# Kernel optimization log

Hardware: AMD Instinct MI355X
Metric: run time of the kernel (lower is better)

## Reference

```python
import jax, jax.numpy as jnp
import numpy as np
from jax import lax

B, C, H, W = 4, 256, 64, 64
NH, DK, DV = 8, 32, 32
KER, PAD = 3, 1


def conv1x1(x, w, b=None):
    # x: [B,C,H,W], w: [O,C] (1x1 conv kernel), b: [O] or None
    y = jnp.einsum('bchw,oc->bohw', x, w)
    if b is not None:
        y = y + b[None, :, None, None]
    return y


def unfold(x, k, pad):
    # F.unfold equivalent: [B,C,H,W] -> [B, C*k*k, H, W] (channel-major patch order)
    return lax.conv_general_dilated_patches(x, (k, k), (1, 1), [(pad, pad), (pad, pad)])


def local_attention(q, k, v, kernel, pad, n_head):
    # per-head local windowed attention over a kernel x kernel neighborhood
    b, c, h, w = q.shape
    d = c // n_head
    kk = kernel * kernel
    qh = q.reshape(b, n_head, d, h, w)
    kpat = unfold(k, kernel, pad).reshape(b, n_head, d, kk, h, w)
    vpat = unfold(v, kernel, pad).reshape(b, n_head, d, kk, h, w)
    scale = 1.0 / np.sqrt(float(d)).astype(np.float32)
    logits = jnp.einsum('bhdxy,bhdkxy->bhkxy', qh, kpat) * scale
    attn = jax.nn.softmax(logits, axis=2)
    out = jnp.einsum('bhkxy,bhdkxy->bhdxy', attn, vpat)
    return out.reshape(b, c, h, w)


def layernorm2d(x, g, b, eps=1e-6):
    mu = jnp.mean(x, axis=1, keepdims=True)
    var = jnp.mean((x - mu) ** 2, axis=1, keepdims=True)
    return (x - mu) / jnp.sqrt(var + eps) * g[None, :, None, None] + b[None, :, None, None]


def batchnorm2d(x, g, b, eps=1e-5):
    mu = jnp.mean(x, axis=(0, 2, 3), keepdims=True)
    var = jnp.mean((x - mu) ** 2, axis=(0, 2, 3), keepdims=True)
    return (x - mu) / jnp.sqrt(var + eps) * g[None, :, None, None] + b[None, :, None, None]


def mha(xq, xkv, wq, wk, wv, wfc, g, bias, kernel, pad):
    residual = xq
    q = conv1x1(xq, wq)
    k = conv1x1(xkv, wk)
    v = conv1x1(xkv, wv)
    o = local_attention(q, k, v, kernel, pad, NH)
    o = conv1x1(o, wfc) + residual
    return layernorm2d(o, g, bias)


def ffn(x, w1, b1, w2, b2, g, bias):
    residual = x
    y = conv1x1(jax.nn.relu(conv1x1(x, w1, b1)), w2, b2)
    y = batchnorm2d(y, g, bias)
    return y + residual


def setup_inputs() -> dict:
    key = jax.random.key(0)
    ks = jax.random.split(key, 16)
    s = 0.05
    d = {
        'input1': jax.random.normal(ks[0], (B, C, H, W), jnp.float32),
        'input2': jax.random.normal(ks[1], (B, C, H, W), jnp.float32),
        'slf_wq': jax.random.normal(ks[2], (NH * DK, C), jnp.float32) * s,
        'slf_wk': jax.random.normal(ks[3], (NH * DK, C), jnp.float32) * s,
        'slf_wv': jax.random.normal(ks[4], (NH * DV, C), jnp.float32) * s,
        'slf_fc': jax.random.normal(ks[5], (C, NH * DV), jnp.float32) * s,
        'slf_g': jnp.ones((C,), jnp.float32),
        'slf_b': jnp.zeros((C,), jnp.float32),
        'crs_wq': jax.random.normal(ks[6], (NH * DK, C), jnp.float32) * s,
        'crs_wk': jax.random.normal(ks[7], (NH * DK, C), jnp.float32) * s,
        'crs_wv': jax.random.normal(ks[8], (NH * DV, C), jnp.float32) * s,
        'crs_fc': jax.random.normal(ks[9], (C, NH * DV), jnp.float32) * s,
        'crs_g': jnp.ones((C,), jnp.float32),
        'crs_b': jnp.zeros((C,), jnp.float32),
        'ffn_w1': jax.random.normal(ks[10], (C, C), jnp.float32) * s,
        'ffn_b1': jnp.zeros((C,), jnp.float32),
        'ffn_w2': jax.random.normal(ks[11], (C, C), jnp.float32) * s,
        'ffn_b2': jnp.zeros((C,), jnp.float32),
        'ffn_bn_g': jnp.ones((C,), jnp.float32),
        'ffn_bn_b': jnp.zeros((C,), jnp.float32),
        'kernel': KER,
        'pad': PAD,
    }
    return d


def reference(input1, input2, slf_wq, slf_wk, slf_wv, slf_fc, slf_g, slf_b,
              crs_wq, crs_wk, crs_wv, crs_fc, crs_g, crs_b,
              ffn_w1, ffn_b1, ffn_w2, ffn_b2, ffn_bn_g, ffn_bn_b, kernel, pad):
    slf1 = mha(input1, input1, slf_wq, slf_wk, slf_wv, slf_fc, slf_g, slf_b, kernel, pad)
    slf2 = mha(input2, input2, slf_wq, slf_wk, slf_wv, slf_fc, slf_g, slf_b, kernel, pad)
    crs1 = mha(slf1, slf2, crs_wq, crs_wk, crs_wv, crs_fc, crs_g, crs_b, kernel, pad)
    crs2 = mha(slf2, slf1, crs_wq, crs_wk, crs_wv, crs_fc, crs_g, crs_b, kernel, pad)
    out1 = ffn(crs1, ffn_w1, ffn_b1, ffn_w2, ffn_b2, ffn_bn_g, ffn_bn_b)
    out2 = ffn(crs2, ffn_w1, ffn_b1, ffn_w2, ffn_b2, ffn_bn_g, ffn_bn_b)
    return (out1, out2)
```

## Files before the change

### kernel.cpp

```cpp
#include <hip/hip_runtime.h>
#include <stdint.h>

using u16 = unsigned short;
typedef __bf16 bf16x8 __attribute__((ext_vector_type(8)));
typedef __bf16 bf16x2 __attribute__((ext_vector_type(2)));
typedef float f32x4 __attribute__((ext_vector_type(4)));

#define NPIX 16384
#define CDIM 256

__device__ __forceinline__ float b2f(u16 u) {
  union { unsigned i; float f; } c; c.i = ((unsigned)u) << 16; return c.f;
}
__device__ __forceinline__ u16 f2b(float x) {
  union { __bf16 h; u16 u; } c; c.h = (__bf16)x; return c.u;
}
__device__ __forceinline__ unsigned pack2(float a, float b) {
  union { bf16x2 v; unsigned u; } c; c.v[0] = (__bf16)a; c.v[1] = (__bf16)b; return c.u;
}
__device__ __forceinline__ void unpack8(uint4 w, float* f) {
  f[0] = b2f((u16)(w.x & 0xffffu)); f[1] = b2f((u16)(w.x >> 16));
  f[2] = b2f((u16)(w.y & 0xffffu)); f[3] = b2f((u16)(w.y >> 16));
  f[4] = b2f((u16)(w.z & 0xffffu)); f[5] = b2f((u16)(w.z >> 16));
  f[6] = b2f((u16)(w.w & 0xffffu)); f[7] = b2f((u16)(w.w >> 16));
}

__device__ __forceinline__ void async16(u16* l, const u16* g) {
  __builtin_amdgcn_global_load_lds((const __attribute__((address_space(1))) void*)g,
                                   (__attribute__((address_space(3))) void*)l, 16, 0, 0);
}

template <int NI, int NT>
__device__ __forceinline__ void stage_swz(u16* lds, const u16* src, int tid) {
#pragma unroll
  for (int i = 0; i < NI; ++i) {
    const int idx = i * NT + tid;
    const int row = idx >> 3;
    const int c8 = (idx & 7) ^ (row & 7);
    async16(lds + idx * 8, src + (size_t)row * 256 + c8 * 8);
  }
}

__device__ __forceinline__ void compute_tile(const u16* ab, const u16* bb,
                                             f32x4 (&acc)[4][4], int wr, int wc,
                                             int l15, int l4, int sw) {
#pragma unroll
  for (int kk = 0; kk < 2; ++kk) {
    const int cs = ((kk * 4 + l4) ^ sw) * 8;
    bf16x8 af[4], bfr[4];
#pragma unroll
    for (int mi = 0; mi < 4; ++mi)
      af[mi] = *(const bf16x8*)&ab[(wr * 64 + mi * 16 + l15) * 64 + cs];
#pragma unroll
    for (int ni = 0; ni < 4; ++ni)
      bfr[ni] = *(const bf16x8*)&bb[(wc * 64 + ni * 16 + l15) * 64 + cs];
#pragma unroll
    for (int mi = 0; mi < 4; ++mi)
#pragma unroll
      for (int ni = 0; ni < 4; ++ni)
        acc[mi][ni] = __builtin_amdgcn_mfma_f32_16x16x32_bf16(af[mi], bfr[ni],
                                                              acc[mi][ni], 0, 0, 0);
  }
}

__global__ void prep(const float* __restrict__ x1, const float* __restrict__ x2,
                     u16* __restrict__ X1, u16* __restrict__ X2,
                     const float* s0, const float* s1, const float* s2,
                     const float* s3, const float* s4, const float* s5,
                     const float* s6, const float* s7, const float* s8,
                     const float* s9, u16* __restrict__ wdst,
                     float* __restrict__ stats) {
  const int t = threadIdx.x;
  const int yy = blockIdx.y;
  if (yy >= 32) {
    const int m = yy - 32;
    if (m == 0 && blockIdx.x == 0) {
      ((float4*)stats)[t] = float4{0.f, 0.f, 0.f, 0.f};
    }
    const float* s;
    switch (m) {
      case 0: s = s0; break; case 1: s = s1; break; case 2: s = s2; break;
      case 3: s = s3; break; case 4: s = s4; break; case 5: s = s5; break;
      case 6: s = s6; break; case 7: s = s7; break; case 8: s = s8; break;
      default: s = s9; break;
    }
    const int i = (blockIdx.x * 256 + t) * 4;
    float4 v = *(const float4*)(s + i);
    uint2 o;
    o.x = pack2(v.x, v.y);
    o.y = pack2(v.z, v.w);
    *(uint2*)(wdst + (size_t)m * 65536 + i) = o;
    return;
  }
  __shared__ u16 tile[64][65];
  const int z = yy >> 2;
  const float* x = (z < 4) ? x1 : x2;
  u16* X = (z < 4) ? X1 : X2;
  const int b = z & 3, c0 = (yy & 3) * 64, hw0 = blockIdx.x * 64;
  {
    const int hw_l = t & 63, cb = t >> 6;
#pragma unroll
    for (int i = 0; i < 16; ++i) {
      const int c_l = cb * 16 + i;
      tile[c_l][hw_l] = f2b(x[((size_t)(b * 256 + c0 + c_l)) * 4096 + hw0 + hw_l]);
    }
  }
  __syncthreads();
  {
    const int c_l = t & 63, hb = t >> 6;
#pragma unroll
    for (int i = 0; i < 16; ++i) {
      const int hw_l = hb * 16 + i;
      X[((size_t)(b * 4096 + hw0 + hw_l)) * 256 + c0 + c_l] = tile[c_l][hw_l];
    }
  }
}

struct PG { const u16* X[6]; const u16* W[3]; u16* D[6]; };

template <int NG>
__global__ void gemm_qkv(PG a) {
  __shared__ u16 As[2][8192];
  __shared__ u16 Bs[2][8192];
  const int tid = threadIdx.x;
  const int wave = tid >> 6, lane = tid & 63;
  const int p0 = blockIdx.x * 128;
  const int g = blockIdx.y >> 1, o0 = (blockIdx.y & 1) * 128;
  const int z = blockIdx.z;
  const u16* X = a.X[z * NG + g];
  const u16* W = a.W[g];
  u16* D = a.D[z * NG + g];
  const int wr = wave & 1, wc = wave >> 1;
  const int l15 = lane & 15, l4 = lane >> 4;
  const int sw = l15 & 7;
  f32x4 acc[4][4] = {};

  const u16* Xp = X + (size_t)p0 * 256;
  const u16* Wp = W + (size_t)o0 * 256;
  stage_swz<4, 256>(As[0], Xp, tid);
  stage_swz<4, 256>(Bs[0], Wp, tid);
  __syncthreads();

  for (int kt = 0; kt < 4; ++kt) {
    const int cur = kt & 1;
    if (kt < 3) {
      stage_swz<4, 256>(As[cur ^ 1], Xp + (kt + 1) * 64, tid);
      stage_swz<4, 256>(Bs[cur ^ 1], Wp + (kt + 1) * 64, tid);
    }
    compute_tile(As[cur], Bs[cur], acc, wr, wc, l15, l4, sw);
    __syncthreads();
  }
#pragma unroll
  for (int ni = 0; ni < 4; ++ni) {
    const int o = o0 + wc * 64 + ni * 16 + l15;
#pragma unroll
    for (int mi = 0; mi < 4; ++mi)
#pragma unroll
      for (int r = 0; r < 4; ++r) {
        const int p = p0 + wr * 64 + mi * 16 + l4 * 4 + r;
        D[(size_t)p * 256 + o] = f2b(acc[mi][ni][r]);
      }
  }
}

struct Pas { const u16* Q[2]; const u16* K[2]; const u16* V[2];
             const u16* res[2]; u16* dstS[2]; u16* dstQc[2];
             const u16* Wfc; const u16* Wcq; const float* g; const float* b; };

__global__ __launch_bounds__(512) void attn_s(Pas a) {
  __shared__ u16 A4[2][8192];
  __shared__ u16 Bs[16384];
  __shared__ u16 S4[4][8192];
  __shared__ float red[2][128][4];
  const int tid = threadIdx.x;
  const int wave = tid >> 6, lane = tid & 63;
  const int wr = wave & 1, wc = wave >> 1;
  const int l15 = lane & 15, l4 = lane >> 4;
  const int sw = l15 & 7;
  const int p0 = blockIdx.x * 128;
  const int z = blockIdx.y;
  const u16* __restrict__ Q = a.Q[z];
  const u16* __restrict__ K = a.K[z];
  const u16* __restrict__ V = a.V[z];
  const u16* __restrict__ res = a.res[z];
  u16* dstS = a.dstS[z];
  u16* dstQc = a.dstQc[z];

  const int p_l = tid >> 2, hh = tid & 3;
  const int p = p0 + p_l;
  const int yq = (p >> 6) & 63, xq = p & 63;

  bool inb[9];
  ptrdiff_t noff[9];
#pragma unroll
  for (int j = 0; j < 9; ++j) {
    const int dy = j / 3 - 1, dx = j % 3 - 1;
    inb[j] = ((unsigned)(yq + dy) < 64u) && ((unsigned)(xq + dx) < 64u);
    noff[j] = (ptrdiff_t)(dy * 64 + dx) * 256;
  }

  stage_swz<4, 512>(Bs, a.Wfc, tid);
  __builtin_amdgcn_sched_barrier(0);

  f32x4 acc[4][4] = {};
  for (int h = 0; h < 2; ++h) {
    const int head = h * 4 + hh;
    const size_t base = (size_t)p * 256 + head * 32;
    float q[32];
    {
      const uint4* qp = (const uint4*)(Q + base);
#pragma unroll
      for (int i = 0; i < 4; ++i) { uint4 w = qp[i]; unpack8(w, q + i * 8); }
    }
    float accj[9];
#pragma unroll
    for (int j = 0; j < 9; ++j) accj[j] = 0.f;
#pragma unroll
    for (int i = 0; i < 4; ++i) {
      uint4 w[9];
#pragma unroll
      for (int j = 0; j < 9; ++j)
        if (inb[j]) w[j] = ((const uint4*)(K + base + noff[j]))[i];
#pragma unroll
      for (int j = 0; j < 9; ++j) {
        if (inb[j]) {
          float kf[8]; unpack8(w[j], kf);
#pragma unroll
          for (int d = 0; d < 8; ++d) accj[j] += q[i * 8 + d] * kf[d];
        }
      }
    }
    float lg[9];
    float mx = -1e30f;
#pragma unroll
    for (int j = 0; j < 9; ++j) {
      const float l = inb[j] ? accj[j] * 0.17677669529663687f : 0.f;
      lg[j] = l;
      mx = fmaxf(mx, l);
    }
    float pr[9], den = 0.f;
#pragma unroll
    for (int j = 0; j < 9; ++j) { pr[j] = __expf(lg[j] - mx); den += pr[j]; }
    float out[32];
#pragma unroll
    for (int d = 0; d < 32; ++d) out[d] = 0.f;
#pragma unroll
    for (int i = 0; i < 4; ++i) {
      uint4 w[9];
#pragma unroll
      for (int j = 0; j < 9; ++j)
        if (inb[j]) w[j] = ((const uint4*)(V + base + noff[j]))[i];
#pragma unroll
      for (int j = 0; j < 9; ++j) {
        if (inb[j]) {
          float vf[8]; unpack8(w[j], vf);
          const float pw = pr[j];
#pragma unroll
          for (int d = 0; d < 8; ++d) out[i * 8 + d] += pw * vf[d];
        }
      }
    }
    const float inv = 1.f / den;
#pragma unroll
    for (int i = 0; i < 4; ++i) {
      uint4 w;
      w.x = pack2(out[i * 8 + 0] * inv, out[i * 8 + 1] * inv);
      w.y = pack2(out[i * 8 + 2] * inv, out[i * 8 + 3] * inv);
      w.z = pack2(out[i * 8 + 4] * inv, out[i * 8 + 5] * inv);
      w.w = pack2(out[i * 8 + 6] * inv, out[i * 8 + 7] * inv);
      const int c8g = hh * 4 + i;
      const int sub = c8g >> 3, c8in = c8g & 7;
      *(uint4*)&A4[sub][p_l * 64 + ((c8in ^ (p_l & 7)) * 8)] = w;
    }

    __syncthreads();
    compute_tile(A4[0], Bs, acc, wr, wc, l15, l4, sw);
    __syncthreads();
    stage_swz<4, 512>(Bs, a.Wfc + (h * 2 + 1) * 64, tid);
    __syncthreads();
    compute_tile(A4[1], Bs, acc, wr, wc, l15, l4, sw);
    __syncthreads();
    if (h == 0) {
      stage_swz<4, 512>(Bs, a.Wfc + 2 * 64, tid);
      __builtin_amdgcn_sched_barrier(0);
    }
  }

  stage_swz<4, 512>(Bs, a.Wcq, tid);
  __builtin_amdgcn_sched_barrier(0);

#pragma unroll
  for (int mi = 0; mi < 4; ++mi) {
#pragma unroll
    for (int r = 0; r < 4; ++r) {
      const int pl = wr * 64 + mi * 16 + l4 * 4 + r;
      const int pp = p0 + pl;
      float s = 0.f, s2 = 0.f;
#pragma unroll
      for (int ni = 0; ni < 4; ++ni) {
        const int o = wc * 64 + ni * 16 + l15;
        float vv = acc[mi][ni][r] + b2f(res[(size_t)pp * 256 + o]);
        acc[mi][ni][r] = vv;
        s += vv; s2 += vv * vv;
      }
#pragma unroll
      for (int m = 1; m < 16; m <<= 1) {
        s += __shfl_xor(s, m); s2 += __shfl_xor(s2, m);
      }
      if (l15 == 0) { red[0][pl][wc] = s; red[1][pl][wc] = s2; }
    }
  }
  __syncthreads();

  float gv[4], bv[4];
#pragma unroll
  for (int ni = 0; ni < 4; ++ni) {
    const int o = wc * 64 + ni * 16 + l15;
    gv[ni] = a.g[o]; bv[ni] = a.b[o];
  }
#pragma unroll
  for (int mi = 0; mi < 4; ++mi) {
#pragma unroll
    for (int r = 0; r < 4; ++r) {
      const int pl = wr * 64 + mi * 16 + l4 * 4 + r;
      const float st = red[0][pl][0] + red[0][pl][1] + red[0][pl][2] + red[0][pl][3];
      const float s2t = red[1][pl][0] + red[1][pl][1] + red[1][pl][2] + red[1][pl][3];
      const float mu = st * (1.f / 256.f);
      const float var = s2t * (1.f / 256.f) - mu * mu;
      const float inv = rsqrtf(var + 1e-6f);
      const int pp = p0 + pl;
#pragma unroll
      for (int ni = 0; ni < 4; ++ni) {
        const int o = wc * 64 + ni * 16 + l15;
        const u16 hv = f2b((acc[mi][ni][r] - mu) * inv * gv[ni] + bv[ni]);
        dstS[(size_t)pp * 256 + o] = hv;
        const int c8 = (ni * 16 + l15) >> 3;
        S4[wc][pl * 64 + ((c8 ^ (pl & 7)) * 8) + (l15 & 7)] = hv;
      }
    }
  }
  __syncthreads();

  u16* a4f = &A4[0][0];
  f32x4 accq[4][4] = {};
  for (int kt = 0; kt < 4; ++kt) {
    if (kt < 3)
      stage_swz<4, 512>(((kt + 1) & 1) ? a4f : Bs, a.Wcq + (kt + 1) * 64, tid);
    compute_tile(&S4[kt][0], (kt & 1) ? a4f : Bs, accq, wr, wc, l15, l4, sw);
    __syncthreads();
  }
#pragma unroll
  for (int ni = 0; ni < 4; ++ni) {
    const int o = wc * 64 + ni * 16 + l15;
#pragma unroll
    for (int mi = 0; mi < 4; ++mi)
#pragma unroll
      for (int r = 0; r < 4; ++r) {
        const int pp = p0 + wr * 64 + mi * 16 + l4 * 4 + r;
        dstQc[(size_t)pp * 256 + o] = f2b(accq[mi][ni][r]);
      }
  }
}

struct Pcf { const u16* Q[2]; const u16* K[2]; const u16* V[2];
             const u16* resS[2]; u16* dstC[2]; u16* U[2]; float* st[2];
             const u16* Wfc; const float* g; const float* b;
             const u16* W1; const float* bb1; const u16* W2; const float* bb2; };

__global__ __launch_bounds__(512) void attn_c_ffn(Pcf a) {
  __shared__ u16 A4[2][8192];
  __shared__ u16 Bs[16384];
  __shared__ u16 M4[4][8192];
  __shared__ float red[2][128][4];
  const int tid = threadIdx.x;
  const int wave = tid >> 6, lane = tid & 63;
  const int wr = wave & 1, wc = wave >> 1;
  const int l15 = lane & 15, l4 = lane >> 4;
  const int sw = l15 & 7;
  const int p0 = blockIdx.x * 128;
  const int z = blockIdx.y;
  const u16* __restrict__ Q = a.Q[z];
  const u16* __restrict__ K = a.K[z];
  const u16* __restrict__ V = a.V[z];
  const u16* __restrict__ resS = a.resS[z];
  u16* dstC = a.dstC[z];
  u16* U = a.U[z];
  float* st = a.st[z];

  const int p_l = tid >> 2, hh = tid & 3;
  const int p = p0 + p_l;
  const int yq = (p >> 6) & 63, xq = p & 63;

  bool inb[9];
  ptrdiff_t noff[9];
#pragma unroll
  for (int j = 0; j < 9; ++j) {
    const int dy = j / 3 - 1, dx = j % 3 - 1;
    inb[j] = ((unsigned)(yq + dy) < 64u) && ((unsigned)(xq + dx) < 64u);
    noff[j] = (ptrdiff_t)(dy * 64 + dx) * 256;
  }

  stage_swz<4, 512>(Bs, a.Wfc, tid);
  __builtin_amdgcn_sched_barrier(0);

  f32x4 acc[4][4] = {};
  for (int h = 0; h < 2; ++h) {
    const int head = h * 4 + hh;
    const size_t base = (size_t)p * 256 + head * 32;
    float q[32];
    {
      const uint4* qp = (const uint4*)(Q + base);
#pragma unroll
      for (int i = 0; i < 4; ++i) { uint4 w = qp[i]; unpack8(w, q + i * 8); }
    }
    float accj[9];
#pragma unroll
    for (int j = 0; j < 9; ++j) accj[j] = 0.f;
#pragma unroll
    for (int i = 0; i < 4; ++i) {
      uint4 w[9];
#pragma unroll
      for (int j = 0; j < 9; ++j)
        if (inb[j]) w[j] = ((const uint4*)(K + base + noff[j]))[i];
#pragma unroll
      for (int j = 0; j < 9; ++j) {
        if (inb[j]) {
          float kf[8]; unpack8(w[j], kf);
#pragma unroll
          for (int d = 0; d < 8; ++d) accj[j] += q[i * 8 + d] * kf[d];
        }
      }
    }
    float lg[9];
    float mx = -1e30f;
#pragma unroll
    for (int j = 0; j < 9; ++j) {
      const float l = inb[j] ? accj[j] * 0.17677669529663687f : 0.f;
      lg[j] = l;
      mx = fmaxf(mx, l);
    }
    float pr[9], den = 0.f;
#pragma unroll
    for (int j = 0; j < 9; ++j) { pr[j] = __expf(lg[j] - mx); den += pr[j]; }
    float out[32];
#pragma unroll
    for (int d = 0; d < 32; ++d) out[d] = 0.f;
#pragma unroll
    for (int i = 0; i < 4; ++i) {
      uint4 w[9];
#pragma unroll
      for (int j = 0; j < 9; ++j)
        if (inb[j]) w[j] = ((const uint4*)(V + base + noff[j]))[i];
#pragma unroll
      for (int j = 0; j < 9; ++j) {
        if (inb[j]) {
          float vf[8]; unpack8(w[j], vf);
          const float pw = pr[j];
#pragma unroll
          for (int d = 0; d < 8; ++d) out[i * 8 + d] += pw * vf[d];
        }
      }
    }
    const float inv = 1.f / den;
#pragma unroll
    for (int i = 0; i < 4; ++i) {
      uint4 w;
      w.x = pack2(out[i * 8 + 0] * inv, out[i * 8 + 1] * inv);
      w.y = pack2(out[i * 8 + 2] * inv, out[i * 8 + 3] * inv);
      w.z = pack2(out[i * 8 + 4] * inv, out[i * 8 + 5] * inv);
      w.w = pack2(out[i * 8 + 6] * inv, out[i * 8 + 7] * inv);
      const int c8g = hh * 4 + i;
      const int sub = c8g >> 3, c8in = c8g & 7;
      *(uint4*)&A4[sub][p_l * 64 + ((c8in ^ (p_l & 7)) * 8)] = w;
    }

    __syncthreads();
    compute_tile(A4[0], Bs, acc, wr, wc, l15, l4, sw);
    __syncthreads();
    stage_swz<4, 512>(Bs, a.Wfc + (h * 2 + 1) * 64, tid);
    __syncthreads();
    compute_tile(A4[1], Bs, acc, wr, wc, l15, l4, sw);
    __syncthreads();
    if (h == 0) {
      stage_swz<4, 512>(Bs, a.Wfc + 2 * 64, tid);
      __builtin_amdgcn_sched_barrier(0);
    }
  }

  stage_swz<4, 512>(Bs, a.W1, tid);
  __builtin_amdgcn_sched_barrier(0);

#pragma unroll
  for (int mi = 0; mi < 4; ++mi) {
#pragma unroll
    for (int r = 0; r < 4; ++r) {
      const int pl = wr * 64 + mi * 16 + l4 * 4 + r;
      const int pp = p0 + pl;
      float s = 0.f, s2 = 0.f;
#pragma unroll
      for (int ni = 0; ni < 4; ++ni) {
        const int o = wc * 64 + ni * 16 + l15;
        float vv = acc[mi][ni][r] + b2f(resS[(size_t)pp * 256 + o]);
        acc[mi][ni][r] = vv;
        s += vv; s2 += vv * vv;
      }
#pragma unroll
      for (int m = 1; m < 16; m <<= 1) {
        s += __shfl_xor(s, m); s2 += __shfl_xor(s2, m);
      }
      if (l15 == 0) { red[0][pl][wc] = s; red[1][pl][wc] = s2; }
    }
  }
  __syncthreads();

  float gv[4], bv[4];
#pragma unroll
  for (int ni = 0; ni < 4; ++ni) {
    const int o = wc * 64 + ni * 16 + l15;
    gv[ni] = a.g[o]; bv[ni] = a.b[o];
  }
#pragma unroll
  for (int mi = 0; mi < 4; ++mi) {
#pragma unroll
    for (int r = 0; r < 4; ++r) {
      const int pl = wr * 64 + mi * 16 + l4 * 4 + r;
      const float st2 = red[0][pl][0] + red[0][pl][1] + red[0][pl][2] + red[0][pl][3];
      const float s2t = red[1][pl][0] + red[1][pl][1] + red[1][pl][2] + red[1][pl][3];
      const float mu = st2 * (1.f / 256.f);
      const float var = s2t * (1.f / 256.f) - mu * mu;
      const float inv = rsqrtf(var + 1e-6f);
      const int pp = p0 + pl;
#pragma unroll
      for (int ni = 0; ni < 4; ++ni) {
        const int o = wc * 64 + ni * 16 + l15;
        const u16 hv = f2b((acc[mi][ni][r] - mu) * inv * gv[ni] + bv[ni]);
        dstC[(size_t)pp * 256 + o] = hv;
        const int c8 = (ni * 16 + l15) >> 3;
        M4[wc][pl * 64 + ((c8 ^ (pl & 7)) * 8) + (l15 & 7)] = hv;
      }
    }
  }
  __syncthreads();

  u16* a4f = &A4[0][0];
  f32x4 acc1[4][4] = {};
  for (int kt = 0; kt < 4; ++kt) {
    if (kt < 3)
      stage_swz<4, 512>(((kt + 1) & 1) ? a4f : Bs, a.W1 + (kt + 1) * 64, tid);
    compute_tile(&M4[kt][0], (kt & 1) ? a4f : Bs, acc1, wr, wc, l15, l4, sw);
    __syncthreads();
  }
  stage_swz<4, 512>(Bs, a.W2, tid);
  __builtin_amdgcn_sched_barrier(0);
  {
    float bvv[4];
#pragma unroll
    for (int ni = 0; ni < 4; ++ni) bvv[ni] = a.bb1[wc * 64 + ni * 16 + l15];
    u16* ml = &M4[wc][0];
#pragma unroll
    for (int mi = 0; mi < 4; ++mi) {
#pragma unroll
      for (int r = 0; r < 4; ++r) {
        const int pl = wr * 64 + mi * 16 + l4 * 4 + r;
#pragma unroll
        for (int ni = 0; ni < 4; ++ni) {
          const int col = ni * 16 + l15;
          const int c8 = col >> 3;
          const u16 hv = f2b(fmaxf(acc1[mi][ni][r] + bvv[ni], 0.f));
          ml[pl * 64 + ((c8 ^ (pl & 7)) * 8) + (col & 7)] = hv;
        }
      }
    }
  }
  __syncthreads();

  f32x4 acc2[4][4] = {};
  for (int kt = 0; kt < 4; ++kt) {
    if (kt < 3)
      stage_swz<4, 512>(((kt + 1) & 1) ? a4f : Bs, a.W2 + (kt + 1) * 64, tid);
    compute_tile(&M4[kt][0], (kt & 1) ? a4f : Bs, acc2, wr, wc, l15, l4, sw);
    __syncthreads();
  }
#pragma unroll
  for (int ni = 0; ni < 4; ++ni) {
    const int o = wc * 64 + ni * 16 + l15;
    const float bvv = a.bb2[o];
    float s = 0.f, s2 = 0.f;
#pragma unroll
    for (int mi = 0; mi < 4; ++mi) {
#pragma unroll
      for (int r = 0; r < 4; ++r) {
        const int pp = p0 + wr * 64 + mi * 16 + l4 * 4 + r;
        const u16 hv = f2b(acc2[mi][ni][r] + bvv);
        U[(size_t)pp * 256 + o] = hv;
        const float vr = b2f(hv); s += vr; s2 += vr * vr;
      }
    }
    s += __shfl_xor(s, 16); s2 += __shfl_xor(s2, 16);
    s += __shfl_xor(s, 32); s2 += __shfl_xor(s2, 32);
    if (l4 == 0) { atomicAdd(&st[o], s); atomicAdd(&st[256 + o], s2); }
  }
}

struct Pbn { const u16* U[2]; const u16* res[2]; const float* st[2];
             float* out[2]; const float* g; const float* b; };

__global__ void bn_apply(Pbn a) {
  __shared__ float tile[64][65];
  const int t = threadIdx.x;
  const int s = blockIdx.z >> 2, b = blockIdx.z & 3;
  const u16* __restrict__ U = a.U[s];
  const u16* __restrict__ res = a.res[s];
  const float* st = a.st[s];
  float* out = a.out[s];
  const int c0 = blockIdx.y * 64, hw0 = blockIdx.x * 64;
  {
    const int c_l = t & 63, hb = t >> 6;
    const int c = c0 + c_l;
    const float mu = st[c] * (1.f / 16384.f);
    const float var = st[256 + c] * (1.f / 16384.f) - mu * mu;
    const float sc = rsqrtf(var + 1e-5f) * a.g[c];
    const float sh = a.b[c] - mu * sc;
#pragma unroll
    for (int i = 0; i < 16; ++i) {
      const int hw_l = hb * 16 + i;
      const size_t p = (size_t)b * 4096 + hw0 + hw_l;
      const float u = b2f(U[p * 256 + c]);
      const float r = b2f(res[p * 256 + c]);
      tile[hw_l][c_l] = u * sc + sh + r;
    }
  }
  __syncthreads();
  {
    const int hw_l = t & 63, cb2 = t >> 6;
#pragma unroll
    for (int i = 0; i < 16; ++i) {
      const int c_l = cb2 * 16 + i;
      out[((size_t)(b * 256 + c0 + c_l)) * 4096 + hw0 + hw_l] = tile[hw_l][c_l];
    }
  }
}

extern "C" void kernel_launch(void* const* d_in, const int* in_sizes, int n_in,
                              void* d_out, int out_size, void* d_ws, size_t ws_size,
                              hipStream_t stream) {
  const float* input1 = (const float*)d_in[0];
  const float* input2 = (const float*)d_in[1];
  const float* slf_wq = (const float*)d_in[2];
  const float* slf_wk = (const float*)d_in[3];
  const float* slf_wv = (const float*)d_in[4];
  const float* slf_fc = (const float*)d_in[5];
  const float* slf_g  = (const float*)d_in[6];
  const float* slf_b  = (const float*)d_in[7];
  const float* crs_wq = (const float*)d_in[8];
  const float* crs_wk = (const float*)d_in[9];
  const float* crs_wv = (const float*)d_in[10];
  const float* crs_fc = (const float*)d_in[11];
  const float* crs_g  = (const float*)d_in[12];
  const float* crs_b  = (const float*)d_in[13];
  const float* ffn_w1 = (const float*)d_in[14];
  const float* ffn_b1 = (const float*)d_in[15];
  const float* ffn_w2 = (const float*)d_in[16];
  const float* ffn_b2 = (const float*)d_in[17];
  const float* bn_g   = (const float*)d_in[18];
  const float* bn_b   = (const float*)d_in[19];

  float* out = (float*)d_out;
  u16* ws = (u16*)d_ws;
  const size_t TS = (size_t)NPIX * CDIM;
  u16* b[10];
  for (int i = 0; i < 10; ++i) b[i] = ws + (size_t)i * TS;
  u16* wb = ws + 10 * TS;
  u16 *Wsq = wb,             *Wsk = wb + 65536,     *Wsv = wb + 2 * 65536,
      *Wsf = wb + 3 * 65536, *Wcq = wb + 4 * 65536, *Wck = wb + 5 * 65536,
      *Wcv = wb + 6 * 65536, *Wcf = wb + 7 * 65536, *W1 = wb + 8 * 65536,
      *W2 = wb + 9 * 65536;
  float* stats = (float*)(wb + 10 * 65536);

  const dim3 tb(256);

  prep<<<dim3(64, 42), tb, 0, stream>>>(input1, input2, b[0], b[1],
                                        slf_wq, slf_wk, slf_wv, slf_fc,
                                        crs_wq, crs_wk, crs_wv, crs_fc,
                                        ffn_w1, ffn_w2, wb, stats);

  PG sa;
  sa.X[0] = b[0]; sa.X[1] = b[0]; sa.X[2] = b[0];
  sa.X[3] = b[1]; sa.X[4] = b[1]; sa.X[5] = b[1];
  sa.W[0] = Wsq; sa.W[1] = Wsk; sa.W[2] = Wsv;
  sa.D[0] = b[4]; sa.D[1] = b[5]; sa.D[2] = b[6];
  sa.D[3] = b[7]; sa.D[4] = b[8]; sa.D[5] = b[9];
  gemm_qkv<3><<<dim3(NPIX / 128, 6, 2), tb, 0, stream>>>(sa);

  Pas f1;
  f1.Q[0] = b[4]; f1.K[0] = b[5]; f1.V[0] = b[6];
  f1.Q[1] = b[7]; f1.K[1] = b[8]; f1.V[1] = b[9];
  f1.res[0] = b[0]; f1.res[1] = b[1];
  f1.dstS[0] = b[2]; f1.dstS[1] = b[3];
  f1.dstQc[0] = b[4]; f1.dstQc[1] = b[7];
  f1.Wfc = Wsf; f1.Wcq = Wcq; f1.g = slf_g; f1.b = slf_b;
  attn_s<<<dim3(NPIX / 128, 2), dim3(512), 0, stream>>>(f1);

  PG ca;
  ca.X[0] = b[2]; ca.X[1] = b[2];
  ca.X[2] = b[3]; ca.X[3] = b[3];
  ca.X[4] = nullptr; ca.X[5] = nullptr;
  ca.W[0] = Wck; ca.W[1] = Wcv; ca.W[2] = nullptr;
  ca.D[0] = b[5]; ca.D[1] = b[6];
  ca.D[2] = b[8]; ca.D[3] = b[9];
  ca.D[4] = nullptr; ca.D[5] = nullptr;
  gemm_qkv<2><<<dim3(NPIX / 128, 4, 2), tb, 0, stream>>>(ca);

  Pcf f2;
  f2.Q[0] = b[4]; f2.K[0] = b[8]; f2.V[0] = b[9];
  f2.Q[1] = b[7]; f2.K[1] = b[5]; f2.V[1] = b[6];
  f2.resS[0] = b[2]; f2.resS[1] = b[3];
  f2.dstC[0] = b[0]; f2.dstC[1] = b[1];
  f2.U[0] = b[2]; f2.U[1] = b[3];
  f2.st[0] = stats; f2.st[1] = stats + 512;
  f2.Wfc = Wcf; f2.g = crs_g; f2.b = crs_b;
  f2.W1 = W1; f2.bb1 = ffn_b1; f2.W2 = W2; f2.bb2 = ffn_b2;
  attn_c_ffn<<<dim3(NPIX / 128, 2), dim3(512), 0, stream>>>(f2);

  Pbn bn;
  bn.U[0] = b[2]; bn.U[1] = b[3];
  bn.res[0] = b[0]; bn.res[1] = b[1];
  bn.st[0] = stats; bn.st[1] = stats + 512;
  bn.out[0] = out; bn.out[1] = out + TS;
  bn.g = bn_g; bn.b = bn_b;
  bn_apply<<<dim3(64, 4, 8), tb, 0, stream>>>(bn);
}
```

Baseline: 283.0 us.

## Fuse cross-attention K/V projections into self-attention epilogue kernel

The self-attention kernel already keeps its layernormed output tile in shared memory to compute the cross-attention Q projection. It now also computes the cross-attention K and V projections from that same tile, running the weight staging pipeline across all three weight matrices. This removes the separate gemm_qkv launch for cross K/V, which re-read the self-attention outputs from global memory. The cost is more work per attention block, plus two extra workspace buffers and a reshuffled buffer assignment; whether the original input buffers are free to overwrite in attn_s depends on no other reads of them there.

```diff
diff --git a/kernel.cpp b/kernel.cpp
--- a/kernel.cpp
+++ b/kernel.cpp
@@ -165,7 +165,9 @@
 
 struct Pas { const u16* Q[2]; const u16* K[2]; const u16* V[2];
              const u16* res[2]; u16* dstS[2]; u16* dstQc[2];
-             const u16* Wfc; const u16* Wcq; const float* g; const float* b; };
+             u16* dstKc[2]; u16* dstVc[2];
+             const u16* Wfc; const u16* Wcq; const u16* Wck; const u16* Wcv;
+             const float* g; const float* b; };
 
 __global__ __launch_bounds__(512) void attn_s(Pas a) {
   __shared__ u16 A4[2][8192];
@@ -184,7 +186,6 @@
   const u16* __restrict__ V = a.V[z];
   const u16* __restrict__ res = a.res[z];
   u16* dstS = a.dstS[z];
-  u16* dstQc = a.dstQc[z];
 
   const int p_l = tid >> 2, hh = tid & 3;
   const int p = p0 + p_l;
@@ -342,23 +343,33 @@
   __syncthreads();
 
   u16* a4f = &A4[0][0];
-  f32x4 accq[4][4] = {};
-  for (int kt = 0; kt < 4; ++kt) {
-    if (kt < 3)
-      stage_swz<4, 512>(((kt + 1) & 1) ? a4f : Bs, a.Wcq + (kt + 1) * 64, tid);
-    compute_tile(&S4[kt][0], (kt & 1) ? a4f : Bs, accq, wr, wc, l15, l4, sw);
-    __syncthreads();
-  }
-#pragma unroll
-  for (int ni = 0; ni < 4; ++ni) {
-    const int o = wc * 64 + ni * 16 + l15;
-#pragma unroll
-    for (int mi = 0; mi < 4; ++mi)
-#pragma unroll
-      for (int r = 0; r < 4; ++r) {
-        const int pp = p0 + wr * 64 + mi * 16 + l4 * 4 + r;
-        dstQc[(size_t)pp * 256 + o] = f2b(accq[mi][ni][r]);
-      }
+  const u16* Ws[3] = {a.Wcq, a.Wck, a.Wcv};
+  u16* dsts[3] = {a.dstQc[z], a.dstKc[z], a.dstVc[z]};
+#pragma unroll
+  for (int gq = 0; gq < 3; ++gq) {
+    f32x4 accq[4][4] = {};
+#pragma unroll
+    for (int kt = 0; kt < 4; ++kt) {
+      const int g = gq * 4 + kt;
+      if (g < 11) {
+        const int gn = g + 1;
+        stage_swz<4, 512>((gn & 1) ? a4f : Bs, Ws[gn >> 2] + (gn & 3) * 64, tid);
+      }
+      compute_tile(&S4[kt][0], (g & 1) ? a4f : Bs, accq, wr, wc, l15, l4, sw);
+      __syncthreads();
+    }
+    u16* D = dsts[gq];
+#pragma unroll
+    for (int ni = 0; ni < 4; ++ni) {
+      const int o = wc * 64 + ni * 16 + l15;
+#pragma unroll
+      for (int mi = 0; mi < 4; ++mi)
+#pragma unroll
+        for (int r = 0; r < 4; ++r) {
+          const int pp = p0 + wr * 64 + mi * 16 + l4 * 4 + r;
+          D[(size_t)pp * 256 + o] = f2b(accq[mi][ni][r]);
+        }
+    }
   }
 }
 
@@ -668,9 +679,9 @@
   float* out = (float*)d_out;
   u16* ws = (u16*)d_ws;
   const size_t TS = (size_t)NPIX * CDIM;
-  u16* b[10];
-  for (int i = 0; i < 10; ++i) b[i] = ws + (size_t)i * TS;
-  u16* wb = ws + 10 * TS;
+  u16* b[12];
+  for (int i = 0; i < 12; ++i) b[i] = ws + (size_t)i * TS;
+  u16* wb = ws + 12 * TS;
   u16 *Wsq = wb,             *Wsk = wb + 65536,     *Wsv = wb + 2 * 65536,
       *Wsf = wb + 3 * 65536, *Wcq = wb + 4 * 65536, *Wck = wb + 5 * 65536,
       *Wcv = wb + 6 * 65536, *Wcf = wb + 7 * 65536, *W1 = wb + 8 * 65536,
@@ -698,24 +709,17 @@
   f1.res[0] = b[0]; f1.res[1] = b[1];
   f1.dstS[0] = b[2]; f1.dstS[1] = b[3];
   f1.dstQc[0] = b[4]; f1.dstQc[1] = b[7];
-  f1.Wfc = Wsf; f1.Wcq = Wcq; f1.g = slf_g; f1.b = slf_b;
+  f1.dstKc[0] = b[0]; f1.dstKc[1] = b[1];
+  f1.dstVc[0] = b[10]; f1.dstVc[1] = b[11];
+  f1.Wfc = Wsf; f1.Wcq = Wcq; f1.Wck = Wck; f1.Wcv = Wcv;
+  f1.g = slf_g; f1.b = slf_b;
   attn_s<<<dim3(NPIX / 128, 2), dim3(512), 0, stream>>>(f1);
 
-  PG ca;
-  ca.X[0] = b[2]; ca.X[1] = b[2];
-  ca.X[2] = b[3]; ca.X[3] = b[3];
-  ca.X[4] = nullptr; ca.X[5] = nullptr;
-  ca.W[0] = Wck; ca.W[1] = Wcv; ca.W[2] = nullptr;
-  ca.D[0] = b[5]; ca.D[1] = b[6];
-  ca.D[2] = b[8]; ca.D[3] = b[9];
-  ca.D[4] = nullptr; ca.D[5] = nullptr;
-  gemm_qkv<2><<<dim3(NPIX / 128, 4, 2), tb, 0, stream>>>(ca);
-
   Pcf f2;
-  f2.Q[0] = b[4]; f2.K[0] = b[8]; f2.V[0] = b[9];
-  f2.Q[1] = b[7]; f2.K[1] = b[5]; f2.V[1] = b[6];
+  f2.Q[0] = b[4]; f2.K[0] = b[1]; f2.V[0] = b[11];
+  f2.Q[1] = b[7]; f2.K[1] = b[0]; f2.V[1] = b[10];
   f2.resS[0] = b[2]; f2.resS[1] = b[3];
-  f2.dstC[0] = b[0]; f2.dstC[1] = b[1];
+  f2.dstC[0] = b[5]; f2.dstC[1] = b[8];
   f2.U[0] = b[2]; f2.U[1] = b[3];
   f2.st[0] = stats; f2.st[1] = stats + 512;
   f2.Wfc = Wcf; f2.g = crs_g; f2.b = crs_b;
@@ -724,7 +728,7 @@
 
   Pbn bn;
   bn.U[0] = b[2]; bn.U[1] = b[3];
-  bn.res[0] = b[0]; bn.res[1] = b[1];
+  bn.res[0] = b[5]; bn.res[1] = b[8];
   bn.st[0] = stats; bn.st[1] = stats + 512;
   bn.out[0] = out; bn.out[1] = out + TS;
   bn.g = bn_g; bn.b = bn_b;
```

Measured after the change: 275.9 us, median of 2. 1.03x faster.
